# Optimization experiments

Measured on AMD Instinct MI355X. Metric: run time of the kernel, lower is better.

The kernel has to match this reference:

```python
import jax, jax.numpy as jnp
import numpy as np
from jax import lax

RADIUS = 0.2
NSAMPLE = 32


def ball_query(radius, nsample, xyz, new_xyz):
    """Vectorized equivalent of the torch nested-loop ball_query.
    xyz: (B,N,3), new_xyz: (B,M,3) -> idx (B,M,nsample) int32.
    Semantics: first `nsample` in-radius indices in ascending order;
    if fewer than nsample, pad with the first valid index; if none, zeros.
    """
    N = xyz.shape[1]
    # squared distances (B,M,N) via ||a||^2 + ||b||^2 - 2 a.b
    dist_sq = (jnp.sum(new_xyz * new_xyz, axis=-1)[:, :, None]
               + jnp.sum(xyz * xyz, axis=-1)[:, None, :]
               - 2.0 * jnp.einsum('bmd,bnd->bmn', new_xyz, xyz))
    mask = dist_sq < (radius * radius)
    # score = point index if in ball else sentinel N; smallest nsample scores
    scores = jnp.where(mask, jnp.arange(N, dtype=jnp.int32), jnp.int32(N))
    neg_vals, _ = lax.top_k(-scores, nsample)   # ascending valid indices first
    cand = -neg_vals                            # (B,M,nsample)
    first = cand[..., :1]                       # first (smallest) valid index or N
    valid = cand < N
    fill = jnp.where(first < N, first, 0)       # pad value (0 if no neighbor)
    return jnp.where(valid, cand, fill)


def group(features, idx):
    # features (B,C,N), idx (B,M,ns) -> (B,C,M,ns)
    return jax.vmap(lambda f, i: f[:, i])(features, idx)


def setup_inputs() -> dict:
    key = jax.random.key(0)
    k1, k2, k3 = jax.random.split(key, 3)
    xyz = jax.random.uniform(k1, (8, 8192, 3), dtype=jnp.float32)
    new_xyz = jax.random.uniform(k2, (8, 2048, 3), dtype=jnp.float32)
    features = jax.random.normal(k3, (8, 128, 8192), dtype=jnp.float32)
    return {"xyz": xyz, "new_xyz": new_xyz, "features": features}


def reference(xyz, new_xyz, features):
    idx = ball_query(RADIUS, NSAMPLE, xyz, new_xyz)          # (B,M,ns)
    xyz_t = jnp.transpose(xyz, (0, 2, 1))                    # (B,3,N)
    grouped_xyz = group(xyz_t, idx)                          # (B,3,M,ns)
    grouped_xyz = grouped_xyz - jnp.transpose(new_xyz, (0, 2, 1))[..., None]
    grouped_features = group(features, idx)                  # (B,C,M,ns)
    # use_xyz=True -> concat along channel dim
    return jnp.concatenate([grouped_xyz, grouped_features], axis=1)
```

## Files before the change

### kernel.cpp

```cpp
#include <hip/hip_runtime.h>

#define B_      8
#define N_      8192
#define M_      2048
#define S_      32
#define C_FEAT  128
#define C_OUT   131
#define G_      8

__device__ float g_ft[(size_t)B_ * N_ * C_FEAT];

typedef float f32x4_t __attribute__((ext_vector_type(4)));
__device__ __forceinline__ void store_nt(float* p, float4 v) {
    f32x4_t x; x.x = v.x; x.y = v.y; x.z = v.z; x.w = v.w;
    __builtin_nontemporal_store(x, (f32x4_t*)p);
}

__global__ __launch_bounds__(256) void transpose_kernel(
    const float* __restrict__ f)
{
    __shared__ float tile[64][68];
    int t = threadIdx.x;
    int n0 = blockIdx.x * 64, c0 = blockIdx.y * 64, b = blockIdx.z;

    int nt = t & 15, cr0 = t >> 4;
    #pragma unroll
    for (int pass = 0; pass < 4; ++pass) {
        int cr = cr0 + pass * 16;
        float4 v = *((const float4*)&f[((size_t)(b * C_FEAT + c0 + cr)) * N_ + n0 + nt * 4]);
        *((float4*)&tile[cr][nt * 4]) = v;
    }
    __syncthreads();
    int ct = t & 15, nr0 = t >> 4;
    #pragma unroll
    for (int pass = 0; pass < 4; ++pass) {
        int nr = nr0 + pass * 16;
        float4 v;
        v.x = tile[ct*4+0][nr];
        v.y = tile[ct*4+1][nr];
        v.z = tile[ct*4+2][nr];
        v.w = tile[ct*4+3][nr];
        *((float4*)&g_ft[((size_t)(b * N_ + n0 + nr)) * C_FEAT + c0 + ct * 4]) = v;
    }
}

__global__ __launch_bounds__(512, 4) void fused_kernel(
    const float* __restrict__ xyz,
    const float* __restrict__ new_xyz,
    float* __restrict__ out)
{
    __shared__ float4 s_sel[G_][S_];
    __shared__ float  s_q[G_][3];
    __shared__ int    s_done[G_];
    __shared__ float  sT[32][256];

    unsigned i = blockIdx.x;
    unsigned b = i & 7u;
    unsigned m0 = (i >> 3) * G_;
    unsigned t = threadIdx.x;
    unsigned w = t >> 6, lane = t & 63u;

    const float* q = new_xyz + ((size_t)(b * M_ + m0 + w)) * 3;
    float qx = q[0], qy = q[1], qz = q[2];
    if (lane == 0) { s_q[w][0] = qx; s_q[w][1] = qy; s_q[w][2] = qz; }
    float qq = __fadd_rn(__fadd_rn(__fmul_rn(qx,qx), __fmul_rn(qy,qy)), __fmul_rn(qz,qz));
    const float* P = xyz + (size_t)b * N_ * 3;

    int done = 0;
    for (int nb = 0; nb < N_ && done < S_; nb += 256) {
        float px[4], py[4], pz[4];
        #pragma unroll
        for (int r = 0; r < 4; ++r) {
            int n = nb + r * 64 + (int)lane;
            px[r] = P[n*3+0]; py[r] = P[n*3+1]; pz[r] = P[n*3+2];
        }
        #pragma unroll
        for (int r = 0; r < 4; ++r) {
            float pp = __fadd_rn(__fadd_rn(__fmul_rn(px[r],px[r]), __fmul_rn(py[r],py[r])), __fmul_rn(pz[r],pz[r]));
            float dt = __fadd_rn(__fadd_rn(__fmul_rn(qz,pz[r]), __fmul_rn(qy,py[r])), __fmul_rn(qx,px[r]));
            float d  = __fsub_rn(__fadd_rn(qq, pp), __fmul_rn(2.0f, dt));
            unsigned long long mk = __ballot(d < 0.04f);
            if ((mk >> lane) & 1ull) {
                int slot = done + __popcll(mk & ((1ull << lane) - 1ull));
                if (slot < S_) {
                    float4 v;
                    v.x = px[r]; v.y = py[r]; v.z = pz[r];
                    v.w = __int_as_float(nb + r * 64 + (int)lane);
                    s_sel[w][slot] = v;
                }
            }
            done += (int)__popcll(mk);
        }
    }
    if (lane == 0) s_done[w] = done;
    __syncthreads();

    if (t < 256) {
        int w2 = (int)(t >> 5), s = (int)(t & 31u);
        int dn = s_done[w2];
        int total = dn < S_ ? dn : S_;
        if (s >= total) {
            float4 v;
            if (dn > 0) v = s_sel[w2][0];
            else { v.x = P[0]; v.y = P[1]; v.z = P[2]; v.w = __int_as_float(0); }
            s_sel[w2][s] = v;
        }
    }
    __syncthreads();

    if (t < 192) {
        unsigned ch = t >> 6, l = t & 63u, qi = l >> 3, s4 = (l & 7u) * 4u;
        float qc = s_q[qi][ch];
        const float* sp = (const float*)&s_sel[qi][0];
        float4 v;
        v.x = __fsub_rn(sp[(s4 + 0) * 4 + ch], qc);
        v.y = __fsub_rn(sp[(s4 + 1) * 4 + ch], qc);
        v.z = __fsub_rn(sp[(s4 + 2) * 4 + ch], qc);
        v.w = __fsub_rn(sp[(s4 + 3) * 4 + ch], qc);
        size_t off = (((size_t)(b * C_OUT + ch)) * M_ + (m0 + qi)) * S_ + s4;
        store_nt(out + off, v);
    }

    unsigned p = t >> 1, h = t & 1u;
    unsigned qg = p >> 5, sg = p & 31u;
    float4 selv = s_sel[qg][sg];
    int n = __float_as_int(selv.w);
    const float* grow = g_ft + ((size_t)(b * N_ + n)) * C_FEAT + h * 16u;

    float4 r0 = ((const float4*)grow)[0];
    float4 r1 = ((const float4*)grow)[1];
    float4 r2 = ((const float4*)grow)[2];
    float4 r3 = ((const float4*)grow)[3];

    for (int k = 0; k < 4; ++k) {
        float4 n0, n1, n2, n3;
        if (k < 3) {
            const float4* src = (const float4*)(grow + (k + 1) * 32);
            n0 = src[0]; n1 = src[1]; n2 = src[2]; n3 = src[3];
        }
        unsigned cb = h * 16u;
        sT[cb +  0][p] = r0.x; sT[cb +  1][p] = r0.y; sT[cb +  2][p] = r0.z; sT[cb +  3][p] = r0.w;
        sT[cb +  4][p] = r1.x; sT[cb +  5][p] = r1.y; sT[cb +  6][p] = r1.z; sT[cb +  7][p] = r1.w;
        sT[cb +  8][p] = r2.x; sT[cb +  9][p] = r2.y; sT[cb + 10][p] = r2.z; sT[cb + 11][p] = r2.w;
        sT[cb + 12][p] = r3.x; sT[cb + 13][p] = r3.y; sT[cb + 14][p] = r3.z; sT[cb + 15][p] = r3.w;
        __syncthreads();
        #pragma unroll
        for (int rep = 0; rep < 4; ++rep) {
            unsigned idx = rep * 512u + t;
            unsigned chl = idx >> 6;
            unsigned l4  = (idx & 63u) * 4u;
            float4 v = *((const float4*)&sT[chl][l4]);
            size_t off = (((size_t)(b * C_OUT + 3 + k * 32 + chl)) * M_ + m0) * S_ + l4;
            store_nt(out + off, v);
        }
        __syncthreads();
        r0 = n0; r1 = n1; r2 = n2; r3 = n3;
    }
}

extern "C" void kernel_launch(void* const* d_in, const int* in_sizes, int n_in,
                              void* d_out, int out_size, void* d_ws, size_t ws_size,
                              hipStream_t stream) {
    const float* xyz      = (const float*)d_in[0];
    const float* new_xyz  = (const float*)d_in[1];
    const float* features = (const float*)d_in[2];
    float* out = (float*)d_out;

    transpose_kernel<<<dim3(N_ / 64, C_FEAT / 64, B_), dim3(256), 0, stream>>>(features);
    fused_kernel<<<dim3(B_ * M_ / G_), dim3(512), 0, stream>>>(xyz, new_xyz, out);
}
```

Baseline: 324.2 us.

## Replace feature transpose with per-channel gather from index buffer

```diff
diff --git a/kernel.cpp b/kernel.cpp
--- a/kernel.cpp
+++ b/kernel.cpp
@@ -6,9 +6,8 @@
 #define S_      32
 #define C_FEAT  128
 #define C_OUT   131
-#define G_      8
 
-__device__ float g_ft[(size_t)B_ * N_ * C_FEAT];
+__device__ int g_idx[(size_t)B_ * M_ * S_];
 
 typedef float f32x4_t __attribute__((ext_vector_type(4)));
 __device__ __forceinline__ void store_nt(float* p, float4 v) {
@@ -16,55 +15,26 @@
     __builtin_nontemporal_store(x, (f32x4_t*)p);
 }
 
-__global__ __launch_bounds__(256) void transpose_kernel(
-    const float* __restrict__ f)
-{
-    __shared__ float tile[64][68];
-    int t = threadIdx.x;
-    int n0 = blockIdx.x * 64, c0 = blockIdx.y * 64, b = blockIdx.z;
-
-    int nt = t & 15, cr0 = t >> 4;
-    #pragma unroll
-    for (int pass = 0; pass < 4; ++pass) {
-        int cr = cr0 + pass * 16;
-        float4 v = *((const float4*)&f[((size_t)(b * C_FEAT + c0 + cr)) * N_ + n0 + nt * 4]);
-        *((float4*)&tile[cr][nt * 4]) = v;
-    }
-    __syncthreads();
-    int ct = t & 15, nr0 = t >> 4;
-    #pragma unroll
-    for (int pass = 0; pass < 4; ++pass) {
-        int nr = nr0 + pass * 16;
-        float4 v;
-        v.x = tile[ct*4+0][nr];
-        v.y = tile[ct*4+1][nr];
-        v.z = tile[ct*4+2][nr];
-        v.w = tile[ct*4+3][nr];
-        *((float4*)&g_ft[((size_t)(b * N_ + n0 + nr)) * C_FEAT + c0 + ct * 4]) = v;
-    }
-}
-
-__global__ __launch_bounds__(512, 4) void fused_kernel(
+__global__ __launch_bounds__(512) void scan_kernel(
     const float* __restrict__ xyz,
     const float* __restrict__ new_xyz,
     float* __restrict__ out)
 {
-    __shared__ float4 s_sel[G_][S_];
-    __shared__ float  s_q[G_][3];
-    __shared__ int    s_done[G_];
-    __shared__ float  sT[32][256];
+    __shared__ float4 s_sel[8][S_];
+    __shared__ float  s_q[8][3];
+    __shared__ int    s_done[8];
 
     unsigned i = blockIdx.x;
     unsigned b = i & 7u;
-    unsigned m0 = (i >> 3) * G_;
+    unsigned m0 = (i >> 3) * 8u;
     unsigned t = threadIdx.x;
     unsigned w = t >> 6, lane = t & 63u;
+    const float* P = xyz + (size_t)b * N_ * 3;
 
     const float* q = new_xyz + ((size_t)(b * M_ + m0 + w)) * 3;
     float qx = q[0], qy = q[1], qz = q[2];
     if (lane == 0) { s_q[w][0] = qx; s_q[w][1] = qy; s_q[w][2] = qz; }
     float qq = __fadd_rn(__fadd_rn(__fmul_rn(qx,qx), __fmul_rn(qy,qy)), __fmul_rn(qz,qz));
-    const float* P = xyz + (size_t)b * N_ * 3;
 
     int done = 0;
     for (int nb = 0; nb < N_ && done < S_; nb += 256) {
@@ -121,40 +91,30 @@
         store_nt(out + off, v);
     }
 
-    unsigned p = t >> 1, h = t & 1u;
-    unsigned qg = p >> 5, sg = p & 31u;
-    float4 selv = s_sel[qg][sg];
-    int n = __float_as_int(selv.w);
-    const float* grow = g_ft + ((size_t)(b * N_ + n)) * C_FEAT + h * 16u;
+    if (t < 256)
+        g_idx[((size_t)(b * M_ + m0)) * S_ + t] = __float_as_int(s_sel[t >> 5][t & 31u].w);
+}
 
-    float4 r0 = ((const float4*)grow)[0];
-    float4 r1 = ((const float4*)grow)[1];
-    float4 r2 = ((const float4*)grow)[2];
-    float4 r3 = ((const float4*)grow)[3];
+__global__ __launch_bounds__(256) void feat_kernel(
+    const float* __restrict__ features,
+    float* __restrict__ out)
+{
+    unsigned i = blockIdx.x;
+    unsigned b = i & 7u;
+    unsigned ch = i >> 3;
+    const float* frow = features + ((size_t)(b * C_FEAT + ch)) * N_;
+    const int4*  idx  = (const int4*)(g_idx + (size_t)b * M_ * S_);
+    float* orow = out + ((size_t)(b * C_OUT + 3 + ch)) * M_ * S_;
 
-    for (int k = 0; k < 4; ++k) {
-        float4 n0, n1, n2, n3;
-        if (k < 3) {
-            const float4* src = (const float4*)(grow + (k + 1) * 32);
-            n0 = src[0]; n1 = src[1]; n2 = src[2]; n3 = src[3];
-        }
-        unsigned cb = h * 16u;
-        sT[cb +  0][p] = r0.x; sT[cb +  1][p] = r0.y; sT[cb +  2][p] = r0.z; sT[cb +  3][p] = r0.w;
-        sT[cb +  4][p] = r1.x; sT[cb +  5][p] = r1.y; sT[cb +  6][p] = r1.z; sT[cb +  7][p] = r1.w;
-        sT[cb +  8][p] = r2.x; sT[cb +  9][p] = r2.y; sT[cb + 10][p] = r2.z; sT[cb + 11][p] = r2.w;
-        sT[cb + 12][p] = r3.x; sT[cb + 13][p] = r3.y; sT[cb + 14][p] = r3.z; sT[cb + 15][p] = r3.w;
-        __syncthreads();
-        #pragma unroll
-        for (int rep = 0; rep < 4; ++rep) {
-            unsigned idx = rep * 512u + t;
-            unsigned chl = idx >> 6;
-            unsigned l4  = (idx & 63u) * 4u;
-            float4 v = *((const float4*)&sT[chl][l4]);
-            size_t off = (((size_t)(b * C_OUT + 3 + k * 32 + chl)) * M_ + m0) * S_ + l4;
-            store_nt(out + off, v);
-        }
-        __syncthreads();
-        r0 = n0; r1 = n1; r2 = n2; r3 = n3;
+    #pragma unroll 4
+    for (unsigned u = threadIdx.x; u < (M_ * S_) / 4; u += 256) {
+        int4 gi = idx[u];
+        float4 v;
+        v.x = frow[gi.x];
+        v.y = frow[gi.y];
+        v.z = frow[gi.z];
+        v.w = frow[gi.w];
+        store_nt(orow + u * 4u, v);
     }
 }
 
@@ -166,6 +126,6 @@
     const float* features = (const float*)d_in[2];
     float* out = (float*)d_out;
 
-    transpose_kernel<<<dim3(N_ / 64, C_FEAT / 64, B_), dim3(256), 0, stream>>>(features);
-    fused_kernel<<<dim3(B_ * M_ / G_), dim3(512), 0, stream>>>(xyz, new_xyz, out);
+    scan_kernel<<<dim3(B_ * M_ / 8), dim3(512), 0, stream>>>(xyz, new_xyz, out);
+    feat_kernel<<<dim3(B_ * C_FEAT), dim3(256), 0, stream>>>(features, out);
 }
```

Measured after the change: 384.7 us. +18.7%, slower.
